# Performance work log

Measured on AMD Instinct MI355X. Metric: run time of the kernel, lower is better.

## Reference

```python
import jax, jax.numpy as jnp
import numpy as np

N_NODES = 100000
N_GRAPHS = 128

def _graph_conv(x, W, b, s, d, n_nodes):
    """DGL GraphConv with norm='both': D_dst^{-1/2} A D_src^{-1/2} X W + b."""
    ones = jnp.ones(s.shape[0], x.dtype)
    deg_out = jax.ops.segment_sum(ones, s, num_segments=n_nodes)  # src out-degree
    deg_in = jax.ops.segment_sum(ones, d, num_segments=n_nodes)   # dst in-degree
    norm_src = jnp.where(deg_out > 0, 1.0 / jnp.sqrt(jnp.maximum(deg_out, 1.0)), 0.0)
    norm_dst = jnp.where(deg_in > 0, 1.0 / jnp.sqrt(jnp.maximum(deg_in, 1.0)), 0.0)
    h = x * norm_src[:, None]                    # [N, F]
    agg = jax.ops.segment_sum(h[s], d, num_segments=n_nodes)  # SpMM gather-scatter
    rst = (agg @ W) * norm_dst[:, None] + b
    return rst

def _hetero_layer(x, Ws, bs, src, dst, n_nodes):
    # HeteroGraphConv aggregate='sum' over relations (fixed small set -> loop ok)
    out = jnp.zeros((n_nodes, Ws.shape[-1]), x.dtype)
    for r in range(Ws.shape[0]):
        out = out + _graph_conv(x, Ws[r], bs[r], src[r], dst[r], n_nodes)
    return out

def setup_inputs() -> dict:
    key = jax.random.key(0)
    ks = jax.random.split(key, 8)
    feat = jax.random.normal(ks[0], (N_NODES, 256), dtype=jnp.float32)
    src = jax.random.randint(ks[1], (3, 400000), 0, N_NODES)
    dst = jax.random.randint(ks[2], (3, 400000), 0, N_NODES)
    graph_ids = jnp.sort(jax.random.randint(ks[3], (N_NODES,), 0, N_GRAPHS))
    W1 = jax.random.normal(ks[4], (3, 256, 256), dtype=jnp.float32) * 0.06
    b1 = jnp.zeros((3, 256), dtype=jnp.float32)
    W2 = jax.random.normal(ks[5], (3, 256, 256), dtype=jnp.float32) * 0.06
    b2 = jnp.zeros((3, 256), dtype=jnp.float32)
    return {"feat": feat, "src": src, "dst": dst, "graph_ids": graph_ids,
            "W1": W1, "b1": b1, "W2": W2, "b2": b2}

def reference(feat, src, dst, graph_ids, W1, b1, W2, b2):
    n_nodes = feat.shape[0]
    h = _hetero_layer(feat, W1, b1, src, dst, n_nodes)
    h = jax.nn.relu(h)
    h = _hetero_layer(h, W2, b2, src, dst, n_nodes)
    # AvgPooling over batched graphs
    sums = jax.ops.segment_sum(h, graph_ids, num_segments=N_GRAPHS)
    counts = jax.ops.segment_sum(jnp.ones(n_nodes, h.dtype), graph_ids, num_segments=N_GRAPHS)
    return sums / jnp.maximum(counts, 1.0)[:, None]
```

## Files before the change

### kernel.cpp

```cpp
#include <hip/hip_runtime.h>
#include <stdint.h>

#define NN 100000
#define NE 400000
#define NR 3
#define NF 256
#define NK 768
#define NG 128
#define SCAN_NB ((NN + 1023) / 1024)

typedef __attribute__((ext_vector_type(4))) unsigned short ushortx4;
typedef __attribute__((ext_vector_type(8))) unsigned short ushortx8;
typedef __attribute__((ext_vector_type(8))) short short8;
typedef __attribute__((ext_vector_type(4))) float floatx4;

static __device__ __forceinline__ unsigned short f2bfu(float f) {
  union { float f; uint32_t u; } c; c.f = f;
  uint32_t x = c.u;
  uint32_t r = (x + 0x7fffu + ((x >> 16) & 1u)) >> 16;
  return (unsigned short)r;
}
static __device__ __forceinline__ float bfu2f(unsigned short u) {
  union { uint32_t u; float f; } c; c.u = ((uint32_t)u) << 16;
  return c.f;
}

static __device__ __forceinline__ void gload16(const void* g, void* l) {
  __builtin_amdgcn_global_load_lds(
      (const __attribute__((address_space(1))) uint32_t*)g,
      (__attribute__((address_space(3))) uint32_t*)l, 16, 0, 0);
}


__global__ __launch_bounds__(256) void degree_kernel(
    const int* __restrict__ src, const int* __restrict__ dst,
    int* __restrict__ deg_out, int* __restrict__ deg_in) {
  int t = blockIdx.x * 256 + threadIdx.x;
  int r = blockIdx.y;
  if (t < NE) {
    atomicAdd(&deg_out[r * NN + src[r * NE + t]], 1);
    atomicAdd(&deg_in[r * NN + dst[r * NE + t]], 1);
  }
}

__global__ __launch_bounds__(128) void gcount_kernel(
    const int* __restrict__ gid, int* __restrict__ gcount) {
  int g = threadIdx.x;
  int lo = 0, hi = NN;
  while (lo < hi) { int mid = (lo + hi) >> 1; if (gid[mid] < g) lo = mid + 1; else hi = mid; }
  int a = lo;
  lo = 0; hi = NN;
  while (lo < hi) { int mid = (lo + hi) >> 1; if (gid[mid] < g + 1) lo = mid + 1; else hi = mid; }
  gcount[g] = lo - a;
}

__global__ __launch_bounds__(256) void norm_kernel(
    const int* __restrict__ deg_out, const int* __restrict__ deg_in,
    float* __restrict__ n_src, float* __restrict__ n_dst) {
  int t = blockIdx.x * 256 + threadIdx.x;
  if (t < NR * NN) {
    int dof = deg_out[t], din = deg_in[t];
    n_src[t] = dof > 0 ? rsqrtf((float)dof) : 0.f;
    n_dst[t] = din > 0 ? rsqrtf((float)din) : 0.f;
  }
}


__global__ __launch_bounds__(256) void scan_phaseA(
    const int* __restrict__ deg_in, int* __restrict__ blocksum) {
  int r = blockIdx.y, b = blockIdx.x, tid = threadIdx.x;
  const int* deg = deg_in + (size_t)r * NN;
  int base = b * 1024 + tid * 4;
  int s = 0;
#pragma unroll
  for (int i = 0; i < 4; ++i) { int idx = base + i; if (idx < NN) s += deg[idx]; }
  __shared__ int red[256];
  red[tid] = s; __syncthreads();
  for (int off = 128; off > 0; off >>= 1) {
    if (tid < off) red[tid] += red[tid + off];
    __syncthreads();
  }
  if (tid == 0) blocksum[r * SCAN_NB + b] = red[0];
}

__global__ __launch_bounds__(128) void scan_phaseB(
    int* __restrict__ blocksum, int* __restrict__ rowptr) {
  int r = blockIdx.x, tid = threadIdx.x;
  int* bs = blocksum + r * SCAN_NB;
  __shared__ int buf[128];
  int v = (tid < SCAN_NB) ? bs[tid] : 0;
  buf[tid] = v; __syncthreads();
  for (int off = 1; off < 128; off <<= 1) {
    int t = (tid >= off) ? buf[tid - off] : 0;
    __syncthreads();
    buf[tid] += t;
    __syncthreads();
  }
  if (tid < SCAN_NB) bs[tid] = buf[tid] - v;
  if (tid == 127) rowptr[(size_t)r * (NN + 1) + NN] = buf[127];
}

__global__ __launch_bounds__(256) void scan_phaseC(
    const int* __restrict__ deg_in, const int* __restrict__ blocksum,
    int* __restrict__ rowptr) {
  int r = blockIdx.y, b = blockIdx.x, tid = threadIdx.x;
  const int* deg = deg_in + (size_t)r * NN;
  int* rp = rowptr + (size_t)r * (NN + 1);
  int base = b * 1024 + tid * 4;
  int v[4]; int s = 0;
#pragma unroll
  for (int i = 0; i < 4; ++i) { int idx = base + i; v[i] = (idx < NN) ? deg[idx] : 0; s += v[i]; }
  __shared__ int buf[256];
  buf[tid] = s; __syncthreads();
  for (int off = 1; off < 256; off <<= 1) {
    int t = (tid >= off) ? buf[tid - off] : 0;
    __syncthreads();
    buf[tid] += t;
    __syncthreads();
  }
  int excl = buf[tid] - s + blocksum[r * SCAN_NB + b];
#pragma unroll
  for (int i = 0; i < 4; ++i) {
    int idx = base + i;
    if (idx < NN) rp[idx] = excl;
    excl += v[i];
  }
}

__global__ __launch_bounds__(256) void scatter_kernel(
    const int* __restrict__ src, const int* __restrict__ dst,
    int* __restrict__ cursor, const float* __restrict__ n_src,
    int2* __restrict__ csr_e) {
  int t = blockIdx.x * 256 + threadIdx.x;
  int r = blockIdx.y;
  if (t < NE) {
    int s = src[r * NE + t], v = dst[r * NE + t];
    int pos = atomicAdd(&cursor[r * (NN + 1) + v], 1);
    csr_e[(size_t)r * NE + pos] = make_int2(s, __float_as_int(n_src[r * NN + s]));
  }
}


__global__ __launch_bounds__(256) void prep_w_kernel(
    const float* __restrict__ W1, const float* __restrict__ W2,
    unsigned short* __restrict__ wt1, unsigned short* __restrict__ wt2) {
  __shared__ float lds[64][65];
  const int tile = blockIdx.x;
  const int r = blockIdx.y;
  const int lay = blockIdx.z;
  const float* W = lay ? W2 : W1;
  unsigned short* wt = lay ? wt2 : wt1;
  const int k0 = (tile >> 2) * 64, n0 = (tile & 3) * 64;
  const int ty = threadIdx.x >> 6;
  const int tx = threadIdx.x & 63;

#pragma unroll
  for (int i = 0; i < 16; ++i) {
    int kl = ty * 16 + i;
    lds[kl][tx] = W[((size_t)r * NF + k0 + kl) * NF + n0 + tx];
  }
  __syncthreads();
#pragma unroll
  for (int i = 0; i < 16; ++i) {
    int nl = ty * 16 + i;
    wt[(size_t)(n0 + nl) * NK + r * NF + k0 + tx] = f2bfu(lds[tx][nl]);
  }
}

__global__ __launch_bounds__(256) void prep_bias_kernel(
    const float* __restrict__ b1, const float* __restrict__ b2,
    float* __restrict__ bs1, float* __restrict__ bs2) {
  int t = blockIdx.x * 256 + threadIdx.x;
  if (t < 2 * NF) {
    int lay = t / NF, n = t % NF;
    const float* b = lay ? b2 : b1;
    float* bs = lay ? bs2 : bs1;
    bs[n] = b[n] + b[NF + n] + b[2 * NF + n];
  }
}

__global__ __launch_bounds__(256) void cast_kernel(
    const float* __restrict__ in, unsigned short* __restrict__ out, int n4) {
  int t = blockIdx.x * 256 + threadIdx.x;
  if (t < n4) {
    floatx4 v = __builtin_nontemporal_load((const floatx4*)&in[(size_t)t * 4]);
    ushortx4 o;
    o.x = f2bfu(v.x); o.y = f2bfu(v.y); o.z = f2bfu(v.z); o.w = f2bfu(v.w);
    *(ushortx4*)&out[(size_t)t * 4] = o;
  }
}


__global__ __launch_bounds__(256) void spmm_kernel(
    const unsigned short* __restrict__ x,
    const int* __restrict__ rowptr, const int2* __restrict__ csr_e,
    const float* __restrict__ n_dst,
    unsigned short* __restrict__ agg) {
  int wid = threadIdx.x >> 6, l = threadIdx.x & 63;
  int v = blockIdx.x * 4 + wid;
  if (v >= NN) return;
  const int half = l >> 5;
  const int c8 = (l & 31) * 8;

  int ea = rowptr[v],                e1a = rowptr[v + 1];
  int eb = rowptr[(NN + 1) + v],     e1b = rowptr[(NN + 1) + v + 1];
  int ec = rowptr[2 * (NN + 1) + v], e1c = rowptr[2 * (NN + 1) + v + 1];
  const int2* cea = csr_e;
  const int2* ceb = csr_e + (size_t)NE;
  const int2* cec = csr_e + (size_t)2 * NE;

  float a[NR][8];
#pragma unroll
  for (int r = 0; r < NR; ++r)
#pragma unroll
    for (int j = 0; j < 8; ++j) a[r][j] = 0.f;

  while (ea < e1a || eb < e1b || ec < e1c) {
    if (ea < e1a) {
      if (ea + half < e1a) {
        int2 p = cea[ea + half];
        float w = __int_as_float(p.y);
        ushortx8 xv = *(const ushortx8*)&x[(size_t)p.x * NF + c8];
#pragma unroll
        for (int j = 0; j < 8; ++j) a[0][j] += w * bfu2f(xv[j]);
      }
      ea += 2;
    }
    if (eb < e1b) {
      if (eb + half < e1b) {
        int2 p = ceb[eb + half];
        float w = __int_as_float(p.y);
        ushortx8 xv = *(const ushortx8*)&x[(size_t)p.x * NF + c8];
#pragma unroll
        for (int j = 0; j < 8; ++j) a[1][j] += w * bfu2f(xv[j]);
      }
      eb += 2;
    }
    if (ec < e1c) {
      if (ec + half < e1c) {
        int2 p = cec[ec + half];
        float w = __int_as_float(p.y);
        ushortx8 xv = *(const ushortx8*)&x[(size_t)p.x * NF + c8];
#pragma unroll
        for (int j = 0; j < 8; ++j) a[2][j] += w * bfu2f(xv[j]);
      }
      ec += 2;
    }
  }

#pragma unroll
  for (int r = 0; r < NR; ++r)
#pragma unroll
    for (int j = 0; j < 8; ++j) a[r][j] += __shfl_xor(a[r][j], 32);

  if (l < 32) {
#pragma unroll
    for (int r = 0; r < NR; ++r) {
      float nd = n_dst[r * NN + v];
      ushortx8 o;
#pragma unroll
      for (int j = 0; j < 8; ++j) o[j] = f2bfu(a[r][j] * nd);
      *(ushortx8*)&agg[(size_t)v * NK + r * NF + c8] = o;
    }
  }
}


__global__ __launch_bounds__(256, 2) void gemm_kernel(
    const unsigned short* __restrict__ A,
    const unsigned short* __restrict__ Bt,
    const float* __restrict__ bias,
    unsigned short* __restrict__ C,
    int M, int relu) {
  __shared__ unsigned short ldsA[2][128 * 32];
  __shared__ unsigned short ldsB[2][256 * 32];
  const int tid = threadIdx.x;
  const int l = tid & 63, wid = tid >> 6;
  const int row0 = blockIdx.x * 128;
  const int c0 = wid * 64;

  floatx4 acc[8][4];
#pragma unroll
  for (int i = 0; i < 8; ++i)
#pragma unroll
    for (int j = 0; j < 4; ++j)
#pragma unroll
      for (int q = 0; q < 4; ++q) acc[i][j][q] = 0.f;

  const int fr = l & 15, fk = (l >> 4) * 8;

  auto stage = [&](int b, int kt) {
    const int k0 = kt * 32;
    int u = wid * 64 + l;
    int arow = row0 + (u >> 2);
    if (arow >= M) arow = M - 1;
    gload16(A + (size_t)arow * NK + k0 + (u & 3) * 8, &ldsA[b][u * 8]);
    u += 256;
    arow = row0 + (u >> 2);
    if (arow >= M) arow = M - 1;
    gload16(A + (size_t)arow * NK + k0 + (u & 3) * 8, &ldsA[b][u * 8]);
#pragma unroll
    for (int p = 0; p < 4; ++p) {
      int uu = p * 256 + wid * 64 + l;
      gload16(Bt + (size_t)(uu >> 2) * NK + k0 + (uu & 3) * 8, &ldsB[b][uu * 8]);
    }
  };

  stage(0, 0);
  asm volatile("s_waitcnt vmcnt(0)" ::: "memory");
  __syncthreads();

  int cur = 0;
  for (int kt = 0; kt < NK / 32; ++kt) {
    if (kt + 1 < NK / 32) stage(cur ^ 1, kt + 1);

    short8 af[8], bf[4];
#pragma unroll
    for (int m = 0; m < 8; ++m)
      af[m] = *(const short8*)&ldsA[cur][(m * 16 + fr) * 32 + fk];
#pragma unroll
    for (int n = 0; n < 4; ++n)
      bf[n] = *(const short8*)&ldsB[cur][(c0 + n * 16 + fr) * 32 + fk];
#pragma unroll
    for (int m = 0; m < 8; ++m)
#pragma unroll
      for (int n = 0; n < 4; ++n)
        acc[m][n] = __builtin_amdgcn_mfma_f32_16x16x32_bf16(af[m], bf[n], acc[m][n], 0, 0, 0);

    asm volatile("s_waitcnt vmcnt(0)" ::: "memory");
    __syncthreads();
    cur ^= 1;
  }

  const int fq = l >> 4;
#pragma unroll
  for (int m = 0; m < 8; ++m) {
#pragma unroll
    for (int n = 0; n < 4; ++n) {
      int col = c0 + n * 16 + fr;
      float bv = bias[col];
#pragma unroll
      for (int q = 0; q < 4; ++q) {
        int row = row0 + m * 16 + fq * 4 + q;
        if (row < M) {
          float vv = acc[m][n][q] + bv;
          if (relu) vv = fmaxf(vv, 0.f);
          C[(size_t)row * NF + col] = f2bfu(vv);
        }
      }
    }
  }
}


__global__ __launch_bounds__(256) void pool_kernel(
    const unsigned short* __restrict__ h2, const int* __restrict__ gid,
    float* __restrict__ poolsum) {
  int c = threadIdx.x;
  int v0 = blockIdx.x * 256;
  int vend = min(v0 + 256, NN);
  float acc = 0.f;
  int curg = -1;
  for (int v = v0; v < vend; ++v) {
    int g = gid[v];
    if (g != curg) {
      if (curg >= 0) atomicAdd(&poolsum[curg * NF + c], acc);
      curg = g; acc = 0.f;
    }
    acc += bfu2f(h2[(size_t)v * NF + c]);
  }
  if (curg >= 0) atomicAdd(&poolsum[curg * NF + c], acc);
}

__global__ __launch_bounds__(256) void final_kernel(
    const float* __restrict__ poolsum, const int* __restrict__ gcount,
    float* __restrict__ out) {
  int g = blockIdx.x, c = threadIdx.x;
  out[g * NF + c] = poolsum[g * NF + c] / fmaxf((float)gcount[g], 1.f);
}


extern "C" void kernel_launch(void* const* d_in, const int* in_sizes, int n_in,
                              void* d_out, int out_size, void* d_ws, size_t ws_size,
                              hipStream_t stream) {
  const float* feat = (const float*)d_in[0];
  const int* src = (const int*)d_in[1];
  const int* dst = (const int*)d_in[2];
  const int* gid = (const int*)d_in[3];
  const float* W1 = (const float*)d_in[4];
  const float* b1 = (const float*)d_in[5];
  const float* W2 = (const float*)d_in[6];
  const float* b2 = (const float*)d_in[7];
  float* out = (float*)d_out;

  char* ws = (char*)d_ws;
  size_t off = 0;
  auto alloc = [&](size_t bytes) -> void* {
    void* p = ws + off;
    off = (off + bytes + 255) & ~(size_t)255;
    return p;
  };

  int* deg_out = (int*)alloc((size_t)NR * NN * 4);
  int* deg_in  = (int*)alloc((size_t)NR * NN * 4);
  float* poolsum = (float*)alloc((size_t)NG * NF * 4);
  size_t zero_bytes = off;

  int* cursor  = (int*)alloc((size_t)NR * (NN + 1) * 4);
  int* gcount  = (int*)alloc((size_t)NG * 4);
  int* blocksum = (int*)alloc((size_t)NR * SCAN_NB * 4);
  float* n_src = (float*)alloc((size_t)NR * NN * 4);
  float* n_dst = (float*)alloc((size_t)NR * NN * 4);
  int* rowptr  = (int*)alloc((size_t)NR * (NN + 1) * 4);
  int2* csr_e  = (int2*)alloc((size_t)NR * NE * 8);
  unsigned short* wt1 = (unsigned short*)alloc((size_t)NF * NK * 2);
  unsigned short* wt2 = (unsigned short*)alloc((size_t)NF * NK * 2);
  float* bs1 = (float*)alloc(NF * 4);
  float* bs2 = (float*)alloc(NF * 4);
  unsigned short* featbf = (unsigned short*)alloc((size_t)NN * NF * 2);
  unsigned short* h1 = (unsigned short*)alloc((size_t)NN * NF * 2);
  unsigned short* h2 = (unsigned short*)alloc((size_t)NN * NF * 2);
  unsigned short* agg = (unsigned short*)alloc((size_t)NN * NK * 2);
  (void)ws_size; (void)in_sizes; (void)n_in; (void)out_size;

  hipMemsetAsync(d_ws, 0, zero_bytes, stream);

  dim3 eg((NE + 255) / 256, NR);
  degree_kernel<<<eg, 256, 0, stream>>>(src, dst, deg_out, deg_in);
  gcount_kernel<<<1, 128, 0, stream>>>(gid, gcount);
  norm_kernel<<<(NR * NN + 255) / 256, 256, 0, stream>>>(deg_out, deg_in, n_src, n_dst);
  scan_phaseA<<<dim3(SCAN_NB, NR), 256, 0, stream>>>(deg_in, blocksum);
  scan_phaseB<<<NR, 128, 0, stream>>>(blocksum, rowptr);
  scan_phaseC<<<dim3(SCAN_NB, NR), 256, 0, stream>>>(deg_in, blocksum, rowptr);
  hipMemcpyAsync(cursor, rowptr, (size_t)NR * (NN + 1) * 4,
                 hipMemcpyDeviceToDevice, stream);
  scatter_kernel<<<eg, 256, 0, stream>>>(src, dst, cursor, n_src, csr_e);

  prep_w_kernel<<<dim3(16, NR, 2), 256, 0, stream>>>(W1, W2, wt1, wt2);
  prep_bias_kernel<<<2, 256, 0, stream>>>(b1, b2, bs1, bs2);
  cast_kernel<<<(NN * NF / 4 + 255) / 256, 256, 0, stream>>>(feat, featbf, NN * NF / 4);

  spmm_kernel<<<(NN + 3) / 4, 256, 0, stream>>>(featbf, rowptr, csr_e, n_dst, agg);
  gemm_kernel<<<(NN + 127) / 128, 256, 0, stream>>>(agg, wt1, bs1, h1, NN, 1);
  spmm_kernel<<<(NN + 3) / 4, 256, 0, stream>>>(h1, rowptr, csr_e, n_dst, agg);
  gemm_kernel<<<(NN + 127) / 128, 256, 0, stream>>>(agg, wt2, bs2, h2, NN, 0);
  pool_kernel<<<(NN + 255) / 256, 256, 0, stream>>>(h2, gid, poolsum);
  final_kernel<<<NG, 256, 0, stream>>>(poolsum, gcount, out);
}
```

Before: 724.3 us.

## Load GEMM MFMA fragments directly from global memory instead of LDS staging

The GEMM kernel drops its double-buffered LDS staging via global_load_lds and instead has each wave load its A and B MFMA fragments straight from global memory into registers, with the k-loop unrolled by four. This removes the LDS traffic and the per-iteration barriers. In exchange, the four waves in a block each load the same A rows separately and rely on cache for that reuse, and there is no explicit prefetch of the next k tile, so load latency may be exposed.

```diff
diff --git a/kernel.cpp b/kernel.cpp
--- a/kernel.cpp
+++ b/kernel.cpp
@@ -23,12 +23,6 @@
 static __device__ __forceinline__ float bfu2f(unsigned short u) {
   union { uint32_t u; float f; } c; c.u = ((uint32_t)u) << 16;
   return c.f;
-}
-
-static __device__ __forceinline__ void gload16(const void* g, void* l) {
-  __builtin_amdgcn_global_load_lds(
-      (const __attribute__((address_space(1))) uint32_t*)g,
-      (__attribute__((address_space(3))) uint32_t*)l, 16, 0, 0);
 }
 
 
@@ -272,64 +266,44 @@
     const float* __restrict__ bias,
     unsigned short* __restrict__ C,
     int M, int relu) {
-  __shared__ unsigned short ldsA[2][128 * 32];
-  __shared__ unsigned short ldsB[2][256 * 32];
-  const int tid = threadIdx.x;
-  const int l = tid & 63, wid = tid >> 6;
+  const int l = threadIdx.x & 63, wid = threadIdx.x >> 6;
   const int row0 = blockIdx.x * 128;
   const int c0 = wid * 64;
+  const int fr = l & 15, fk = (l >> 4) * 8;
+
+  const unsigned short* arow[8];
+#pragma unroll
+  for (int m = 0; m < 8; ++m) {
+    int r = row0 + m * 16 + fr;
+    if (r >= M) r = M - 1;
+    arow[m] = A + (size_t)r * NK + fk;
+  }
+  const unsigned short* brow[4];
+#pragma unroll
+  for (int n = 0; n < 4; ++n)
+    brow[n] = Bt + (size_t)(c0 + n * 16 + fr) * NK + fk;
 
   floatx4 acc[8][4];
 #pragma unroll
-  for (int i = 0; i < 8; ++i)
-#pragma unroll
-    for (int j = 0; j < 4; ++j)
-#pragma unroll
-      for (int q = 0; q < 4; ++q) acc[i][j][q] = 0.f;
-
-  const int fr = l & 15, fk = (l >> 4) * 8;
-
-  auto stage = [&](int b, int kt) {
-    const int k0 = kt * 32;
-    int u = wid * 64 + l;
-    int arow = row0 + (u >> 2);
-    if (arow >= M) arow = M - 1;
-    gload16(A + (size_t)arow * NK + k0 + (u & 3) * 8, &ldsA[b][u * 8]);
-    u += 256;
-    arow = row0 + (u >> 2);
-    if (arow >= M) arow = M - 1;
-    gload16(A + (size_t)arow * NK + k0 + (u & 3) * 8, &ldsA[b][u * 8]);
-#pragma unroll
-    for (int p = 0; p < 4; ++p) {
-      int uu = p * 256 + wid * 64 + l;
-      gload16(Bt + (size_t)(uu >> 2) * NK + k0 + (uu & 3) * 8, &ldsB[b][uu * 8]);
-    }
-  };
-
-  stage(0, 0);
-  asm volatile("s_waitcnt vmcnt(0)" ::: "memory");
-  __syncthreads();
-
-  int cur = 0;
+  for (int m = 0; m < 8; ++m)
+#pragma unroll
+    for (int n = 0; n < 4; ++n)
+#pragma unroll
+      for (int q = 0; q < 4; ++q) acc[m][n][q] = 0.f;
+
+#pragma unroll 4
   for (int kt = 0; kt < NK / 32; ++kt) {
-    if (kt + 1 < NK / 32) stage(cur ^ 1, kt + 1);
-
+    const int ko = kt * 32;
     short8 af[8], bf[4];
 #pragma unroll
-    for (int m = 0; m < 8; ++m)
-      af[m] = *(const short8*)&ldsA[cur][(m * 16 + fr) * 32 + fk];
-#pragma unroll
-    for (int n = 0; n < 4; ++n)
-      bf[n] = *(const short8*)&ldsB[cur][(c0 + n * 16 + fr) * 32 + fk];
+    for (int m = 0; m < 8; ++m) af[m] = *(const short8*)(arow[m] + ko);
+#pragma unroll
+    for (int n = 0; n < 4; ++n) bf[n] = *(const short8*)(brow[n] + ko);
 #pragma unroll
     for (int m = 0; m < 8; ++m)
 #pragma unroll
       for (int n = 0; n < 4; ++n)
         acc[m][n] = __builtin_amdgcn_mfma_f32_16x16x32_bf16(af[m], bf[n], acc[m][n], 0, 0, 0);
-
-    asm volatile("s_waitcnt vmcnt(0)" ::: "memory");
-    __syncthreads();
-    cur ^= 1;
   }
 
   const int fq = l >> 4;
```

New measurement: 864.3 us. +19.3%, slower.
